# Optimization experiments

Measured on AMD Instinct MI355X. Metric: run time of the kernel, lower is better.

## Reference

```python
import jax, jax.numpy as jnp
import numpy as np

B, V, D, K = 32, 4096, 64, 512


def setup_inputs() -> dict:
    key = jax.random.key(0)
    k1, k2 = jax.random.split(key)
    z_e = jax.random.normal(k1, (B, V, D), dtype=jnp.float32)
    # nn.Embedding weight initialized uniform(-1/K, 1/K)
    emb = jax.random.uniform(k2, (K, D), dtype=jnp.float32, minval=-1.0 / K, maxval=1.0 / K)
    return {"z_e": z_e, "emb": emb}


def reference(z_e, emb):
    b, v, d = z_e.shape
    flat = z_e.reshape(-1, d)  # [N, D], N = B*V
    # Squared Euclidean distances via dot-product expansion.
    # torch.cdist returns sqrt of this, but argmin is identical (monotone sqrt).
    d2 = (
        jnp.sum(flat * flat, axis=-1, keepdims=True)  # [N, 1]
        - 2.0 * flat @ emb.T                          # [N, K]
        + jnp.sum(emb * emb, axis=-1)                 # [K]
    )
    indices = jnp.argmin(d2, axis=1)                  # [N]
    z_q = emb[indices].reshape(z_e.shape)             # [B, V, D]
    z_q_st = z_e + jax.lax.stop_gradient(z_q - z_e)   # straight-through
    return z_q_st, z_q, indices.reshape(b, v)
```

## Files before the change

### kernel.cpp

```cpp
#include <hip/hip_runtime.h>


#define VQ_N (32 * 4096)
#define VQ_D 64
#define VQ_K 512

__device__ __forceinline__ float freeze(float x) {
  asm volatile("" : "+v"(x));
  return x;
}

__global__ __launch_bounds__(256) void vq_norms_kernel(
    const float* __restrict__ emb, float* __restrict__ nrm) {
  int k = blockIdx.x * blockDim.x + threadIdx.x;
  if (k < VQ_K) {
    const float* e = emb + k * VQ_D;
    float r0 = freeze(e[0] * e[0]), r1 = freeze(e[1] * e[1]);
    float r2 = freeze(e[2] * e[2]), r3 = freeze(e[3] * e[3]);
    float r4 = freeze(e[4] * e[4]), r5 = freeze(e[5] * e[5]);
    float r6 = freeze(e[6] * e[6]), r7 = freeze(e[7] * e[7]);
#pragma unroll
    for (int i = 8; i < VQ_D; i += 8) {
      r0 += freeze(e[i + 0] * e[i + 0]); r1 += freeze(e[i + 1] * e[i + 1]);
      r2 += freeze(e[i + 2] * e[i + 2]); r3 += freeze(e[i + 3] * e[i + 3]);
      r4 += freeze(e[i + 4] * e[i + 4]); r5 += freeze(e[i + 5] * e[i + 5]);
      r6 += freeze(e[i + 6] * e[i + 6]); r7 += freeze(e[i + 7] * e[i + 7]);
    }
    nrm[k] = ((r0 + r1) + (r2 + r3)) + ((r4 + r5) + (r6 + r7));
  }
}

__global__ __launch_bounds__(256) void vq_main_kernel(
    const float* __restrict__ z_e, const float* __restrict__ emb,
    const float* __restrict__ nrm, float* __restrict__ out_st,
    float* __restrict__ out_q, float* __restrict__ out_idx) {
  __shared__ float s_val[256];
  __shared__ int s_idx[256];
  __shared__ int s_best[64];

  const int tid = threadIdx.x;
  const int lane = tid & 63;
  const int chunk = __builtin_amdgcn_readfirstlane(tid >> 6);
  const int row = blockIdx.x * 64 + lane;

  float z[VQ_D];
  const float4* z4 = (const float4*)(z_e + (size_t)row * VQ_D);
#pragma unroll
  for (int j = 0; j < 16; ++j) {
    float4 v = z4[j];
    z[4 * j + 0] = v.x; z[4 * j + 1] = v.y;
    z[4 * j + 2] = v.z; z[4 * j + 3] = v.w;
  }

  float r0 = freeze(z[0] * z[0]), r1 = freeze(z[1] * z[1]);
  float r2 = freeze(z[2] * z[2]), r3 = freeze(z[3] * z[3]);
  float r4 = freeze(z[4] * z[4]), r5 = freeze(z[5] * z[5]);
  float r6 = freeze(z[6] * z[6]), r7 = freeze(z[7] * z[7]);
#pragma unroll
  for (int i = 8; i < VQ_D; i += 8) {
    r0 += freeze(z[i + 0] * z[i + 0]); r1 += freeze(z[i + 1] * z[i + 1]);
    r2 += freeze(z[i + 2] * z[i + 2]); r3 += freeze(z[i + 3] * z[i + 3]);
    r4 += freeze(z[i + 4] * z[i + 4]); r5 += freeze(z[i + 5] * z[i + 5]);
    r6 += freeze(z[i + 6] * z[i + 6]); r7 += freeze(z[i + 7] * z[i + 7]);
  }
  const float A = ((r0 + r1) + (r2 + r3)) + ((r4 + r5) + (r6 + r7));

  const int k0 = chunk * (VQ_K / 4);
  float bestv = 3.4e38f;
  int best = k0;
  for (int kk = k0; kk < k0 + VQ_K / 4; kk += 4) {
#pragma unroll
    for (int d = 0; d < VQ_D; ++d) asm volatile("" : "+v"(z[d]));

    const float* e0 = emb + (size_t)(kk + 0) * VQ_D;
    const float* e1 = emb + (size_t)(kk + 1) * VQ_D;
    const float* e2 = emb + (size_t)(kk + 2) * VQ_D;
    const float* e3 = emb + (size_t)(kk + 3) * VQ_D;
    float a0 = 0.f, a1 = 0.f, a2 = 0.f, a3 = 0.f;
#pragma unroll
    for (int d = 0; d < VQ_D; ++d) {
      a0 = fmaf(z[d], e0[d], a0);
      a1 = fmaf(z[d], e1[d], a1);
      a2 = fmaf(z[d], e2[d], a2);
      a3 = fmaf(z[d], e3[d], a3);
    }
    float t0 = fmaf(-2.0f, a0, A) + nrm[kk + 0];
    float t1 = fmaf(-2.0f, a1, A) + nrm[kk + 1];
    float t2 = fmaf(-2.0f, a2, A) + nrm[kk + 2];
    float t3 = fmaf(-2.0f, a3, A) + nrm[kk + 3];
    if (t0 < bestv) { bestv = t0; best = kk + 0; }
    if (t1 < bestv) { bestv = t1; best = kk + 1; }
    if (t2 < bestv) { bestv = t2; best = kk + 2; }
    if (t3 < bestv) { bestv = t3; best = kk + 3; }
  }

  s_val[chunk * 64 + lane] = bestv;
  s_idx[chunk * 64 + lane] = best;
  __syncthreads();

  if (tid < 64) {
    float v = s_val[tid];
    int b = s_idx[tid];
#pragma unroll
    for (int c = 1; c < 4; ++c) {
      float vc = s_val[c * 64 + tid];
      if (vc < v) { v = vc; b = s_idx[c * 64 + tid]; }
    }
    s_best[tid] = b;
    out_idx[row] = (float)b;
  }
  __syncthreads();

  const float4* e4 = (const float4*)emb;
  const size_t base4 = (size_t)blockIdx.x * 64 * 16;
  float4* o0 = (float4*)out_st;
  float4* o1 = (float4*)out_q;
#pragma unroll
  for (int t = 0; t < 4; ++t) {
    int i = t * 256 + tid;
    int r = i >> 4, j = i & 15;
    float4 v = e4[s_best[r] * 16 + j];
    o0[base4 + i] = v;
    o1[base4 + i] = v;
  }
}

extern "C" void kernel_launch(void* const* d_in, const int* in_sizes, int n_in,
                              void* d_out, int out_size, void* d_ws,
                              size_t ws_size, hipStream_t stream) {
  const float* z_e = (const float*)d_in[0];
  const float* emb = (const float*)d_in[1];
  float* nrm = (float*)d_ws;

  float* out_st = (float*)d_out;
  float* out_q = out_st + (size_t)VQ_N * VQ_D;
  float* out_idx = out_q + (size_t)VQ_N * VQ_D;

  vq_norms_kernel<<<(VQ_K + 255) / 256, 256, 0, stream>>>(emb, nrm);
  vq_main_kernel<<<VQ_N / 64, 256, 0, stream>>>(z_e, emb, nrm, out_st, out_q,
                                                out_idx);
}
```

Measured before the change: 245.5 us.

## Stage z rows in LDS, unroll codebook loop by eight, tile norms kernel

The main kernel now loads the block's 64 z rows cooperatively with coalesced float4 loads into padded shared memory, instead of each thread holding 64 floats in registers. It re-reads z from LDS inside the codebook loop and processes eight codewords per iteration instead of four. This cuts register pressure, which should allow higher occupancy, and raises reuse of each z element. In exchange it adds LDS traffic in the inner loop. The norms kernel also stages embeddings through padded shared memory so its global loads are coalesced.

```diff
diff --git a/kernel.cpp b/kernel.cpp
--- a/kernel.cpp
+++ b/kernel.cpp
@@ -4,36 +4,47 @@
 #define VQ_N (32 * 4096)
 #define VQ_D 64
 #define VQ_K 512
+#define ZSTRIDE 68
 
 __device__ __forceinline__ float freeze(float x) {
   asm volatile("" : "+v"(x));
   return x;
 }
 
-__global__ __launch_bounds__(256) void vq_norms_kernel(
+__global__ __launch_bounds__(64) void vq_norms_kernel(
     const float* __restrict__ emb, float* __restrict__ nrm) {
-  int k = blockIdx.x * blockDim.x + threadIdx.x;
-  if (k < VQ_K) {
-    const float* e = emb + k * VQ_D;
-    float r0 = freeze(e[0] * e[0]), r1 = freeze(e[1] * e[1]);
-    float r2 = freeze(e[2] * e[2]), r3 = freeze(e[3] * e[3]);
-    float r4 = freeze(e[4] * e[4]), r5 = freeze(e[5] * e[5]);
-    float r6 = freeze(e[6] * e[6]), r7 = freeze(e[7] * e[7]);
+  __shared__ float s_e[64 * 65];
+  const int t = threadIdx.x;
+  const float4* src = (const float4*)(emb + (size_t)blockIdx.x * 64 * VQ_D);
 #pragma unroll
-    for (int i = 8; i < VQ_D; i += 8) {
-      r0 += freeze(e[i + 0] * e[i + 0]); r1 += freeze(e[i + 1] * e[i + 1]);
-      r2 += freeze(e[i + 2] * e[i + 2]); r3 += freeze(e[i + 3] * e[i + 3]);
-      r4 += freeze(e[i + 4] * e[i + 4]); r5 += freeze(e[i + 5] * e[i + 5]);
-      r6 += freeze(e[i + 6] * e[i + 6]); r7 += freeze(e[i + 7] * e[i + 7]);
-    }
-    nrm[k] = ((r0 + r1) + (r2 + r3)) + ((r4 + r5) + (r6 + r7));
+  for (int j = 0; j < 16; ++j) {
+    int idx = j * 64 + t;
+    float4 v = src[idx];
+    int r = idx >> 4, c = idx & 15;
+    float* p = s_e + r * 65 + 4 * c;
+    p[0] = v.x; p[1] = v.y; p[2] = v.z; p[3] = v.w;
   }
+  __syncthreads();
+  const float* e = s_e + t * 65;
+  float r0 = freeze(e[0] * e[0]), r1 = freeze(e[1] * e[1]);
+  float r2 = freeze(e[2] * e[2]), r3 = freeze(e[3] * e[3]);
+  float r4 = freeze(e[4] * e[4]), r5 = freeze(e[5] * e[5]);
+  float r6 = freeze(e[6] * e[6]), r7 = freeze(e[7] * e[7]);
+#pragma unroll
+  for (int i = 8; i < VQ_D; i += 8) {
+    r0 += freeze(e[i + 0] * e[i + 0]); r1 += freeze(e[i + 1] * e[i + 1]);
+    r2 += freeze(e[i + 2] * e[i + 2]); r3 += freeze(e[i + 3] * e[i + 3]);
+    r4 += freeze(e[i + 4] * e[i + 4]); r5 += freeze(e[i + 5] * e[i + 5]);
+    r6 += freeze(e[i + 6] * e[i + 6]); r7 += freeze(e[i + 7] * e[i + 7]);
+  }
+  nrm[blockIdx.x * 64 + t] = ((r0 + r1) + (r2 + r3)) + ((r4 + r5) + (r6 + r7));
 }
 
 __global__ __launch_bounds__(256) void vq_main_kernel(
     const float* __restrict__ z_e, const float* __restrict__ emb,
     const float* __restrict__ nrm, float* __restrict__ out_st,
     float* __restrict__ out_q, float* __restrict__ out_idx) {
+  __shared__ float s_z[64 * ZSTRIDE];
   __shared__ float s_val[256];
   __shared__ int s_idx[256];
   __shared__ int s_best[64];
@@ -43,55 +54,84 @@
   const int chunk = __builtin_amdgcn_readfirstlane(tid >> 6);
   const int row = blockIdx.x * 64 + lane;
 
-  float z[VQ_D];
-  const float4* z4 = (const float4*)(z_e + (size_t)row * VQ_D);
+  const float4* zg = (const float4*)(z_e + (size_t)blockIdx.x * 64 * VQ_D);
+#pragma unroll
+  for (int j = 0; j < 4; ++j) {
+    int idx = j * 256 + tid;
+    float4 v = zg[idx];
+    int r = idx >> 4, c = idx & 15;
+    *(float4*)(s_z + r * ZSTRIDE + 4 * c) = v;
+  }
+  __syncthreads();
+
+  const float* zr = s_z + lane * ZSTRIDE;
+
+  float q0 = 0.f, q1 = 0.f, q2 = 0.f, q3 = 0.f;
+  float q4 = 0.f, q5 = 0.f, q6 = 0.f, q7 = 0.f;
 #pragma unroll
   for (int j = 0; j < 16; ++j) {
-    float4 v = z4[j];
-    z[4 * j + 0] = v.x; z[4 * j + 1] = v.y;
-    z[4 * j + 2] = v.z; z[4 * j + 3] = v.w;
+    float4 v = *(const float4*)(zr + 4 * j);
+    if ((j & 1) == 0) {
+      q0 += freeze(v.x * v.x); q1 += freeze(v.y * v.y);
+      q2 += freeze(v.z * v.z); q3 += freeze(v.w * v.w);
+    } else {
+      q4 += freeze(v.x * v.x); q5 += freeze(v.y * v.y);
+      q6 += freeze(v.z * v.z); q7 += freeze(v.w * v.w);
+    }
   }
-
-  float r0 = freeze(z[0] * z[0]), r1 = freeze(z[1] * z[1]);
-  float r2 = freeze(z[2] * z[2]), r3 = freeze(z[3] * z[3]);
-  float r4 = freeze(z[4] * z[4]), r5 = freeze(z[5] * z[5]);
-  float r6 = freeze(z[6] * z[6]), r7 = freeze(z[7] * z[7]);
-#pragma unroll
-  for (int i = 8; i < VQ_D; i += 8) {
-    r0 += freeze(z[i + 0] * z[i + 0]); r1 += freeze(z[i + 1] * z[i + 1]);
-    r2 += freeze(z[i + 2] * z[i + 2]); r3 += freeze(z[i + 3] * z[i + 3]);
-    r4 += freeze(z[i + 4] * z[i + 4]); r5 += freeze(z[i + 5] * z[i + 5]);
-    r6 += freeze(z[i + 6] * z[i + 6]); r7 += freeze(z[i + 7] * z[i + 7]);
-  }
-  const float A = ((r0 + r1) + (r2 + r3)) + ((r4 + r5) + (r6 + r7));
+  const float A = ((q0 + q1) + (q2 + q3)) + ((q4 + q5) + (q6 + q7));
 
   const int k0 = chunk * (VQ_K / 4);
   float bestv = 3.4e38f;
   int best = k0;
-  for (int kk = k0; kk < k0 + VQ_K / 4; kk += 4) {
-#pragma unroll
-    for (int d = 0; d < VQ_D; ++d) asm volatile("" : "+v"(z[d]));
-
+  for (int kk = k0; kk < k0 + VQ_K / 4; kk += 8) {
     const float* e0 = emb + (size_t)(kk + 0) * VQ_D;
     const float* e1 = emb + (size_t)(kk + 1) * VQ_D;
     const float* e2 = emb + (size_t)(kk + 2) * VQ_D;
     const float* e3 = emb + (size_t)(kk + 3) * VQ_D;
+    const float* e4 = emb + (size_t)(kk + 4) * VQ_D;
+    const float* e5 = emb + (size_t)(kk + 5) * VQ_D;
+    const float* e6 = emb + (size_t)(kk + 6) * VQ_D;
+    const float* e7 = emb + (size_t)(kk + 7) * VQ_D;
     float a0 = 0.f, a1 = 0.f, a2 = 0.f, a3 = 0.f;
+    float a4 = 0.f, a5 = 0.f, a6 = 0.f, a7 = 0.f;
 #pragma unroll
-    for (int d = 0; d < VQ_D; ++d) {
-      a0 = fmaf(z[d], e0[d], a0);
-      a1 = fmaf(z[d], e1[d], a1);
-      a2 = fmaf(z[d], e2[d], a2);
-      a3 = fmaf(z[d], e3[d], a3);
+    for (int j = 0; j < 16; ++j) {
+      float4 zv = *(const float4*)(zr + 4 * j);
+      const int d = 4 * j;
+      a0 = fmaf(zv.x, e0[d + 0], a0); a1 = fmaf(zv.x, e1[d + 0], a1);
+      a2 = fmaf(zv.x, e2[d + 0], a2); a3 = fmaf(zv.x, e3[d + 0], a3);
+      a4 = fmaf(zv.x, e4[d + 0], a4); a5 = fmaf(zv.x, e5[d + 0], a5);
+      a6 = fmaf(zv.x, e6[d + 0], a6); a7 = fmaf(zv.x, e7[d + 0], a7);
+      a0 = fmaf(zv.y, e0[d + 1], a0); a1 = fmaf(zv.y, e1[d + 1], a1);
+      a2 = fmaf(zv.y, e2[d + 1], a2); a3 = fmaf(zv.y, e3[d + 1], a3);
+      a4 = fmaf(zv.y, e4[d + 1], a4); a5 = fmaf(zv.y, e5[d + 1], a5);
+      a6 = fmaf(zv.y, e6[d + 1], a6); a7 = fmaf(zv.y, e7[d + 1], a7);
+      a0 = fmaf(zv.z, e0[d + 2], a0); a1 = fmaf(zv.z, e1[d + 2], a1);
+      a2 = fmaf(zv.z, e2[d + 2], a2); a3 = fmaf(zv.z, e3[d + 2], a3);
+      a4 = fmaf(zv.z, e4[d + 2], a4); a5 = fmaf(zv.z, e5[d + 2], a5);
+      a6 = fmaf(zv.z, e6[d + 2], a6); a7 = fmaf(zv.z, e7[d + 2], a7);
+      a0 = fmaf(zv.w, e0[d + 3], a0); a1 = fmaf(zv.w, e1[d + 3], a1);
+      a2 = fmaf(zv.w, e2[d + 3], a2); a3 = fmaf(zv.w, e3[d + 3], a3);
+      a4 = fmaf(zv.w, e4[d + 3], a4); a5 = fmaf(zv.w, e5[d + 3], a5);
+      a6 = fmaf(zv.w, e6[d + 3], a6); a7 = fmaf(zv.w, e7[d + 3], a7);
     }
     float t0 = fmaf(-2.0f, a0, A) + nrm[kk + 0];
     float t1 = fmaf(-2.0f, a1, A) + nrm[kk + 1];
     float t2 = fmaf(-2.0f, a2, A) + nrm[kk + 2];
     float t3 = fmaf(-2.0f, a3, A) + nrm[kk + 3];
+    float t4 = fmaf(-2.0f, a4, A) + nrm[kk + 4];
+    float t5 = fmaf(-2.0f, a5, A) + nrm[kk + 5];
+    float t6 = fmaf(-2.0f, a6, A) + nrm[kk + 6];
+    float t7 = fmaf(-2.0f, a7, A) + nrm[kk + 7];
     if (t0 < bestv) { bestv = t0; best = kk + 0; }
     if (t1 < bestv) { bestv = t1; best = kk + 1; }
     if (t2 < bestv) { bestv = t2; best = kk + 2; }
     if (t3 < bestv) { bestv = t3; best = kk + 3; }
+    if (t4 < bestv) { bestv = t4; best = kk + 4; }
+    if (t5 < bestv) { bestv = t5; best = kk + 5; }
+    if (t6 < bestv) { bestv = t6; best = kk + 6; }
+    if (t7 < bestv) { bestv = t7; best = kk + 7; }
   }
 
   s_val[chunk * 64 + lane] = bestv;
@@ -111,7 +151,7 @@
   }
   __syncthreads();
 
-  const float4* e4 = (const float4*)emb;
+  const float4* e4v = (const float4*)emb;
   const size_t base4 = (size_t)blockIdx.x * 64 * 16;
   float4* o0 = (float4*)out_st;
   float4* o1 = (float4*)out_q;
@@ -119,7 +159,7 @@
   for (int t = 0; t < 4; ++t) {
     int i = t * 256 + tid;
     int r = i >> 4, j = i & 15;
-    float4 v = e4[s_best[r] * 16 + j];
+    float4 v = e4v[s_best[r] * 16 + j];
     o0[base4 + i] = v;
     o1[base4 + i] = v;
   }
@@ -136,7 +176,7 @@
   float* out_q = out_st + (size_t)VQ_N * VQ_D;
   float* out_idx = out_q + (size_t)VQ_N * VQ_D;
 
-  vq_norms_kernel<<<(VQ_K + 255) / 256, 256, 0, stream>>>(emb, nrm);
+  vq_norms_kernel<<<VQ_K / 64, 64, 0, stream>>>(emb, nrm);
   vq_main_kernel<<<VQ_N / 64, 256, 0, stream>>>(z_e, emb, nrm, out_st, out_q,
                                                 out_idx);
 }
```

After: 263.0 us. 1.07x slower.
